# Performance work log

Measured on AMD Instinct MI355X. Metric: run time of the kernel, lower is better.

Reference implementation:

```python
import jax, jax.numpy as jnp
import numpy as np

N = 50000
E = 800000
F_IN = 300
ALPHA = 0.5                      # GCN2Conv alpha
BETA = float(np.log(0.2 / 2.0 + 1.0))  # log(theta/layer + 1), theta=0.2, layer=2
NEG_SLOPE = 0.2                  # GATv2 leaky_relu slope
H, DH = 2, 32                    # GATv2 heads, per-head dim


def _glorot(key, shape):
    s = (6.0 / (shape[0] + shape[-1])) ** 0.5
    return jax.random.uniform(key, shape, jnp.float32, -s, s)


def setup_inputs() -> dict:
    key = jax.random.key(0)
    ks = jax.random.split(key, 24)
    inp = {
        'x': jax.random.normal(ks[0], (N, F_IN), jnp.float32),
        'edge_index': jax.random.randint(ks[1], (2, E), 0, N, dtype=jnp.int32),
        # encoder params
        'W_enc1': _glorot(ks[2], (F_IN, 256)), 'b_enc1': jnp.zeros((256,), jnp.float32),
        'W_enc2': _glorot(ks[3], (256, 256)),                       # GCN2Conv (no bias)
        'W_enc3': _glorot(ks[4], (256, 128)), 'b_enc3': jnp.zeros((128,), jnp.float32),
        'W_enc4': _glorot(ks[5], (128, 64)),  'b_enc4': jnp.zeros((64,), jnp.float32),
        'W_enc5': _glorot(ks[6], (64, 32)),   'b_enc5': jnp.zeros((32,), jnp.float32),
        'Wl_gat': _glorot(ks[7], (32, H * DH)),
        'Wr_gat': _glorot(ks[8], (32, H * DH)),
        'att_gat': _glorot(ks[9], (H, DH)),
        'b_gat': jnp.zeros((H * DH,), jnp.float32),
        # decoder params
        'W_dec1': _glorot(ks[10], (64, 128)),  'b_dec1': jnp.zeros((128,), jnp.float32),
        'W_dec2': _glorot(ks[11], (128, 256)), 'b_dec2': jnp.zeros((256,), jnp.float32),
        'W_dec3': _glorot(ks[12], (256, 256)),                      # GCN2Conv (no bias)
        'W_dec4': _glorot(ks[13], (256, F_IN)), 'b_dec4': jnp.zeros((F_IN,), jnp.float32),
    }
    return inp


def _forward(x, edge_index,
             W_enc1, b_enc1, W_enc2, W_enc3, b_enc3, W_enc4, b_enc4, W_enc5, b_enc5,
             Wl_gat, Wr_gat, att_gat, b_gat,
             W_dec1, b_dec1, W_dec2, b_dec2, W_dec3, W_dec4, b_dec4):
    loops = jnp.arange(N, dtype=edge_index.dtype)
    src = jnp.concatenate([edge_index[0], loops])  # [E+N]
    dst = jnp.concatenate([edge_index[1], loops])
    # symmetric GCN normalization with self-loops (PyG gcn_norm)
    deg = jax.ops.segment_sum(jnp.ones_like(src, jnp.float32), dst, num_segments=N)
    dinv = jnp.where(deg > 0, jax.lax.rsqrt(jnp.maximum(deg, 1e-12)), 0.0)
    norm = dinv[src] * dinv[dst]  # [E+N]

    def prop(h):  # normalized adjacency apply: gather -> scale -> scatter-add
        return jax.ops.segment_sum(h[src] * norm[:, None], dst, num_segments=N)

    def gcn(h, W, b):
        return prop(h @ W) + b

    def gcn2(h, W):  # GCNII with x_0 = layer input, shared weights
        hp = (1.0 - ALPHA) * prop(h) + ALPHA * h
        return (1.0 - BETA) * hp + BETA * (hp @ W)

    def gatv2(h, Wl, Wr, att, b):
        xl = (h @ Wl).reshape(N, H, DH)  # source transform
        xr = (h @ Wr).reshape(N, H, DH)  # target transform
        e = jax.nn.leaky_relu(xl[src] + xr[dst], NEG_SLOPE)  # [E+N, H, DH]
        logits = jnp.einsum('ehd,hd->eh', e, att)            # [E+N, H]
        m = jax.lax.stop_gradient(jax.ops.segment_max(logits, dst, num_segments=N))
        ex = jnp.exp(logits - m[dst])
        den = jax.ops.segment_sum(ex, dst, num_segments=N)
        a = ex / (den[dst] + 1e-16)                          # softmax over in-edges
        out = jax.ops.segment_sum(xl[src] * a[:, :, None], dst, num_segments=N)
        return out.reshape(N, H * DH) + b

    h = gcn(x, W_enc1, b_enc1)
    h = gcn2(h, W_enc2)
    h = gcn(h, W_enc3, b_enc3)
    h = gcn(h, W_enc4, b_enc4)
    h = gcn(h, W_enc5, b_enc5)
    h = gatv2(h, Wl_gat, Wr_gat, att_gat, b_gat)
    h = jax.nn.relu(h)
    h = gcn(h, W_dec1, b_dec1)
    h = gcn(h, W_dec2, b_dec2)
    h = gcn2(h, W_dec3)
    h = gcn(h, W_dec4, b_dec4)
    return jax.nn.sigmoid(h)


def reference(x, edge_index,
              W_enc1, b_enc1, W_enc2, W_enc3, b_enc3, W_enc4, b_enc4, W_enc5, b_enc5,
              Wl_gat, Wr_gat, att_gat, b_gat,
              W_dec1, b_dec1, W_dec2, b_dec2, W_dec3, W_dec4, b_dec4):
    return _forward(x, edge_index,
                    W_enc1, b_enc1, W_enc2, W_enc3, b_enc3, W_enc4, b_enc4, W_enc5, b_enc5,
                    Wl_gat, Wr_gat, att_gat, b_gat,
                    W_dec1, b_dec1, W_dec2, b_dec2, W_dec3, W_dec4, b_dec4)
```

## Files before the change

### kernel.cpp

```cpp
#include <hip/hip_runtime.h>
#include <math.h>

#define NN 50000
#define FIN 300
#define SS 304
constexpr float ALPHA_C = 0.5f;
constexpr float BETA_C  = 0.09531017980432486f;
constexpr float NEG_SLOPE = 0.2f;

typedef unsigned short u16;
typedef __attribute__((ext_vector_type(8))) short short8;
typedef __attribute__((ext_vector_type(4))) float f32x4;
typedef _Float16 hf4 __attribute__((ext_vector_type(4)));

__global__ void hist_kernel(const int* __restrict__ dst, int* __restrict__ deg, int E) {
    int e = blockIdx.x * blockDim.x + threadIdx.x;
    if (e < E) atomicAdd(&deg[dst[e]], 1);
}

__global__ void scan_kernel(const int* __restrict__ deg, int* __restrict__ rowptr, int n) {
    __shared__ int sh[1024];
    __shared__ int carry;
    if (threadIdx.x == 0) { carry = 0; rowptr[0] = 0; }
    __syncthreads();
    for (int base = 0; base < n; base += 1024) {
        int i = base + threadIdx.x;
        int v = (i < n) ? deg[i] : 0;
        sh[threadIdx.x] = v;
        __syncthreads();
        for (int off = 1; off < 1024; off <<= 1) {
            int t = (threadIdx.x >= off) ? sh[threadIdx.x - off] : 0;
            __syncthreads();
            sh[threadIdx.x] += t;
            __syncthreads();
        }
        if (i < n) rowptr[i + 1] = sh[threadIdx.x] + carry;
        __syncthreads();
        if (threadIdx.x == 0) carry += sh[1023];
        __syncthreads();
    }
}

__global__ void dinv_kernel(const int* __restrict__ deg, float* __restrict__ dinv, int n) {
    int i = blockIdx.x * blockDim.x + threadIdx.x;
    if (i < n) dinv[i] = rsqrtf((float)deg[i] + 1.0f);
}

__global__ void copy_int_kernel(const int* __restrict__ a, int* __restrict__ b, int n) {
    int i = blockIdx.x * blockDim.x + threadIdx.x;
    if (i < n) b[i] = a[i];
}

__global__ void fill_kernel(const int* __restrict__ src, const int* __restrict__ dst,
                            const float* __restrict__ dinv, int* __restrict__ cursor,
                            int* __restrict__ csr_src, float* __restrict__ csr_w, int E) {
    int e = blockIdx.x * blockDim.x + threadIdx.x;
    if (e < E) {
        int s = src[e], d = dst[e];
        int p = atomicAdd(&cursor[d], 1);
        csr_src[p] = s;
        csr_w[p]   = dinv[s] * dinv[d];
    }
}

__global__ void splitw_kernel(const float* __restrict__ W, u16* __restrict__ WhT,
                              u16* __restrict__ WlT, int K, int M, int Kp, int total) {
    int t = blockIdx.x * blockDim.x + threadIdx.x;
    if (t >= total) return;
    int c = t / Kp, k = t - c * Kp;
    float x = (c < M && k < K) ? W[(size_t)k * M + c] : 0.f;
    unsigned u = __float_as_uint(x);
    WhT[t] = (u16)(u >> 16);
    float lo = x - __uint_as_float(u & 0xFFFF0000u);
    WlT[t] = (u16)(__float_as_uint(lo) >> 16);
}

__global__ __launch_bounds__(256)
void gemm_mfma_kernel(const float* __restrict__ A, const u16* __restrict__ WhT,
                      const u16* __restrict__ WlT, float* __restrict__ C,
                      _Float16* __restrict__ Cs, int n, int K, int M, int Kp,
                      float cAB, float cA, const float* __restrict__ bias, int gx) {
    __shared__ u16 sAh[64 * 40], sAl[64 * 40], sWh[64 * 40], sWl[64 * 40];
    const int tid = threadIdx.x;
    const int nwg = gridDim.x;
    const int q = nwg >> 3, r = nwg & 7;
    const int xcd = blockIdx.x & 7, off = blockIdx.x >> 3;
    const int wgid = (xcd < r ? xcd * (q + 1) : r * (q + 1) + (xcd - r) * q) + off;
    const int colBase = (wgid % gx) * 64;
    const int rowBase = (wgid / gx) * 64;
    const int lane = tid & 63, wid = tid >> 6;
    const int wr = (wid >> 1) * 32, wc = (wid & 1) * 32;
    const int fr = lane & 15, ko = (lane >> 4) * 8;
    const int wsc = tid >> 2, wsk = (tid & 3) * 8;

    f32x4 acc[2][2] = {};

    for (int k0 = 0; k0 < Kp; k0 += 32) {
        {
            size_t g = (size_t)(colBase + wsc) * Kp + k0 + wsk;
            *(uint4*)&sWh[wsc * 40 + wsk] = *(const uint4*)&WhT[g];
            *(uint4*)&sWl[wsc * 40 + wsk] = *(const uint4*)&WlT[g];
        }
        const bool fullk = (k0 + 32 <= K);
        for (int s = tid; s < 512; s += 256) {
            int rr = s >> 3, kb = (s & 7) * 4;
            int gr = rowBase + rr, kk = k0 + kb;
            float x0 = 0.f, x1 = 0.f, x2 = 0.f, x3 = 0.f;
            if (gr < n) {
                const float* ap = A + (size_t)gr * K + kk;
                if (fullk) { float4 v = *(const float4*)ap; x0 = v.x; x1 = v.y; x2 = v.z; x3 = v.w; }
                else {
                    if (kk     < K) x0 = ap[0];
                    if (kk + 1 < K) x1 = ap[1];
                    if (kk + 2 < K) x2 = ap[2];
                    if (kk + 3 < K) x3 = ap[3];
                }
            }
            unsigned u0 = __float_as_uint(x0), u1 = __float_as_uint(x1);
            unsigned u2 = __float_as_uint(x2), u3 = __float_as_uint(x3);
            uint2 hp; hp.x = (u1 & 0xFFFF0000u) | (u0 >> 16);
                      hp.y = (u3 & 0xFFFF0000u) | (u2 >> 16);
            float l0 = x0 - __uint_as_float(u0 & 0xFFFF0000u);
            float l1 = x1 - __uint_as_float(u1 & 0xFFFF0000u);
            float l2 = x2 - __uint_as_float(u2 & 0xFFFF0000u);
            float l3 = x3 - __uint_as_float(u3 & 0xFFFF0000u);
            uint2 lp; lp.x = (__float_as_uint(l1) & 0xFFFF0000u) | (__float_as_uint(l0) >> 16);
                      lp.y = (__float_as_uint(l3) & 0xFFFF0000u) | (__float_as_uint(l2) >> 16);
            *(uint2*)&sAh[rr * 40 + kb] = hp;
            *(uint2*)&sAl[rr * 40 + kb] = lp;
        }
        __syncthreads();

        short8 ah[2], al[2], bh[2], bl[2];
        ah[0] = *(const short8*)&sAh[(wr +      fr) * 40 + ko];
        ah[1] = *(const short8*)&sAh[(wr + 16 + fr) * 40 + ko];
        al[0] = *(const short8*)&sAl[(wr +      fr) * 40 + ko];
        al[1] = *(const short8*)&sAl[(wr + 16 + fr) * 40 + ko];
        bh[0] = *(const short8*)&sWh[(wc +      fr) * 40 + ko];
        bh[1] = *(const short8*)&sWh[(wc + 16 + fr) * 40 + ko];
        bl[0] = *(const short8*)&sWl[(wc +      fr) * 40 + ko];
        bl[1] = *(const short8*)&sWl[(wc + 16 + fr) * 40 + ko];
#pragma unroll
        for (int i = 0; i < 2; i++)
#pragma unroll
            for (int j = 0; j < 2; j++) {
                acc[i][j] = __builtin_amdgcn_mfma_f32_16x16x32_bf16(al[i], bh[j], acc[i][j], 0, 0, 0);
                acc[i][j] = __builtin_amdgcn_mfma_f32_16x16x32_bf16(ah[i], bl[j], acc[i][j], 0, 0, 0);
                acc[i][j] = __builtin_amdgcn_mfma_f32_16x16x32_bf16(ah[i], bh[j], acc[i][j], 0, 0, 0);
            }
        __syncthreads();
    }

#pragma unroll
    for (int i = 0; i < 2; i++)
#pragma unroll
        for (int j = 0; j < 2; j++) {
            int row0 = rowBase + wr + i * 16 + (lane >> 4) * 4;
            int col  = colBase + wc + j * 16 + fr;
            if (col >= M) continue;
            float bv = bias ? bias[col] : 0.f;
#pragma unroll
            for (int qq = 0; qq < 4; qq++) {
                int rr = row0 + qq;
                if (rr >= n) break;
                float v = cAB * acc[i][j][qq] + bv;
                if (cA != 0.f) v += cA * A[(size_t)rr * K + col];
                C[(size_t)rr * M + col] = v;
                if (Cs) Cs[(size_t)rr * SS + col] = (_Float16)v;
            }
        }
}

__global__ __launch_bounds__(256)
void prop_kernel(const float* __restrict__ h, const _Float16* __restrict__ hs,
                 float* __restrict__ out, _Float16* __restrict__ outs,
                 const int* __restrict__ rowptr, const int* __restrict__ csr_src,
                 const float* __restrict__ csr_w, const float* __restrict__ dinv,
                 const float* __restrict__ bias, int n, int D, float cP, float cH) {
    int wv = (blockIdx.x * blockDim.x + threadIdx.x) >> 6;
    int lane = threadIdx.x & 63;
    int D4 = D >> 2;
    int npw = 64 / D4;
    int sub = lane / D4;
    int cl = lane - sub * D4;
    int i = wv * npw + sub;
    if (i >= n) return;
    int c = cl * 4;
    long bi = (long)i * D4 + cl;
    const float4* h4 = (const float4*)h;
    float4 hv = h4[bi];
    float sw = dinv[i] * dinv[i];
    float4 a0 = {sw * hv.x, sw * hv.y, sw * hv.z, sw * hv.w};
    float4 a1 = {0,0,0,0}, a2 = {0,0,0,0}, a3 = {0,0,0,0};
    int p0 = rowptr[i], p1 = rowptr[i + 1];
    int p = p0;
    for (; p + 4 <= p1; p += 4) {
        int s0 = csr_src[p], s1 = csr_src[p+1], s2 = csr_src[p+2], s3 = csr_src[p+3];
        float w0 = csr_w[p], w1 = csr_w[p+1], w2 = csr_w[p+2], w3 = csr_w[p+3];
        hf4 v0 = *(const hf4*)&hs[(size_t)s0 * SS + c];
        hf4 v1 = *(const hf4*)&hs[(size_t)s1 * SS + c];
        hf4 v2 = *(const hf4*)&hs[(size_t)s2 * SS + c];
        hf4 v3 = *(const hf4*)&hs[(size_t)s3 * SS + c];
        a0.x += w0*(float)v0[0]; a0.y += w0*(float)v0[1]; a0.z += w0*(float)v0[2]; a0.w += w0*(float)v0[3];
        a1.x += w1*(float)v1[0]; a1.y += w1*(float)v1[1]; a1.z += w1*(float)v1[2]; a1.w += w1*(float)v1[3];
        a2.x += w2*(float)v2[0]; a2.y += w2*(float)v2[1]; a2.z += w2*(float)v2[2]; a2.w += w2*(float)v2[3];
        a3.x += w3*(float)v3[0]; a3.y += w3*(float)v3[1]; a3.z += w3*(float)v3[2]; a3.w += w3*(float)v3[3];
    }
    for (; p < p1; ++p) {
        int s = csr_src[p];
        float w = csr_w[p];
        hf4 v = *(const hf4*)&hs[(size_t)s * SS + c];
        a0.x += w*(float)v[0]; a0.y += w*(float)v[1]; a0.z += w*(float)v[2]; a0.w += w*(float)v[3];
    }
    float4 acc = {a0.x + a1.x + a2.x + a3.x, a0.y + a1.y + a2.y + a3.y,
                  a0.z + a1.z + a2.z + a3.z, a0.w + a1.w + a2.w + a3.w};
    float4 rr = {cP * acc.x, cP * acc.y, cP * acc.z, cP * acc.w};
    if (cH != 0.f) { rr.x += cH * hv.x; rr.y += cH * hv.y; rr.z += cH * hv.z; rr.w += cH * hv.w; }
    if (bias) { float4 b = ((const float4*)bias)[cl]; rr.x += b.x; rr.y += b.y; rr.z += b.z; rr.w += b.w; }
    ((float4*)out)[bi] = rr;
    if (outs) {
        hf4 o; o[0] = (_Float16)rr.x; o[1] = (_Float16)rr.y; o[2] = (_Float16)rr.z; o[3] = (_Float16)rr.w;
        *(hf4*)&outs[(size_t)i * SS + c] = o;
    }
}

__device__ inline float lrelu(float x) { return x > 0.f ? x : NEG_SLOPE * x; }

__global__ __launch_bounds__(256)
void gat_logits_kernel(const float* __restrict__ xl, const _Float16* __restrict__ xls,
                       const float* __restrict__ xr, const float* __restrict__ att,
                       const int* __restrict__ rowptr, const int* __restrict__ csr_src,
                       float* __restrict__ logits, float* __restrict__ self_logits, int n) {
    int t = blockIdx.x * blockDim.x + threadIdx.x;
    int i = t >> 1, hh = t & 1;
    if (i >= n) return;
    float4 attv[8], xrv[8];
    const float4* att4 = (const float4*)att;
    const float4* xr4 = (const float4*)xr;
#pragma unroll
    for (int c = 0; c < 8; c++) {
        attv[c] = att4[hh * 8 + c];
        xrv[c]  = xr4[(long)i * 16 + hh * 8 + c];
    }
    {
        const float4* xl4 = (const float4*)xl;
        float s = 0.f;
        long b = (long)i * 16 + hh * 8;
#pragma unroll
        for (int c = 0; c < 8; c++) {
            float4 e = xl4[b + c];
            s += lrelu(e.x + xrv[c].x) * attv[c].x;
            s += lrelu(e.y + xrv[c].y) * attv[c].y;
            s += lrelu(e.z + xrv[c].z) * attv[c].z;
            s += lrelu(e.w + xrv[c].w) * attv[c].w;
        }
        self_logits[i * 2 + hh] = s;
    }
    int p0 = rowptr[i], p1 = rowptr[i + 1];
    for (int p = p0; p < p1; ++p) {
        int sn = csr_src[p];
        size_t b = (size_t)sn * SS + hh * 32;
        float s = 0.f;
#pragma unroll
        for (int c = 0; c < 8; c++) {
            hf4 e = *(const hf4*)&xls[b + c * 4];
            s += lrelu((float)e[0] + xrv[c].x) * attv[c].x;
            s += lrelu((float)e[1] + xrv[c].y) * attv[c].y;
            s += lrelu((float)e[2] + xrv[c].z) * attv[c].z;
            s += lrelu((float)e[3] + xrv[c].w) * attv[c].w;
        }
        logits[(long)p * 2 + hh] = s;
    }
}

__global__ __launch_bounds__(256)
void gat_mden_kernel(const float* __restrict__ logits, const float* __restrict__ self_logits,
                     const int* __restrict__ rowptr, float* __restrict__ m_arr,
                     float* __restrict__ den_arr, int n) {
    int t = blockIdx.x * blockDim.x + threadIdx.x;
    int i = t >> 1, hh = t & 1;
    if (i >= n) return;
    int p0 = rowptr[i], p1 = rowptr[i + 1];
    float m = self_logits[i * 2 + hh];
    for (int p = p0; p < p1; ++p) m = fmaxf(m, logits[(long)p * 2 + hh]);
    float den = expf(self_logits[i * 2 + hh] - m);
    for (int p = p0; p < p1; ++p) den += expf(logits[(long)p * 2 + hh] - m);
    m_arr[i * 2 + hh] = m;
    den_arr[i * 2 + hh] = den;
}

__global__ __launch_bounds__(256)
void gat_out_kernel(const float* __restrict__ xl, const _Float16* __restrict__ xls,
                    const int* __restrict__ rowptr, const int* __restrict__ csr_src,
                    const float* __restrict__ logits, const float* __restrict__ self_logits,
                    const float* __restrict__ m_arr, const float* __restrict__ den_arr,
                    const float* __restrict__ bias, float* __restrict__ out,
                    _Float16* __restrict__ outs, int n) {
    int i = (blockIdx.x * blockDim.x + threadIdx.x) >> 6;
    int lane = threadIdx.x & 63;
    if (i >= n) return;
    int hh = lane >> 5;
    float m = m_arr[i * 2 + hh];
    float inv = 1.f / (den_arr[i * 2 + hh] + 1e-16f);
    float acc = expf(self_logits[i * 2 + hh] - m) * inv * xl[(long)i * 64 + lane];
    int p0 = rowptr[i], p1 = rowptr[i + 1];
    for (int p = p0; p < p1; ++p) {
        float w = expf(logits[(long)p * 2 + hh] - m) * inv;
        acc += w * (float)xls[(size_t)csr_src[p] * SS + lane];
    }
    float r = fmaxf(acc + bias[lane], 0.f);
    out[(long)i * 64 + lane] = r;
    outs[(size_t)i * SS + lane] = (_Float16)r;
}

__global__ void sigmoid_kernel(const float* __restrict__ in, float* __restrict__ out, int n4) {
    int i = blockIdx.x * blockDim.x + threadIdx.x;
    if (i < n4) {
        float4 v = ((const float4*)in)[i];
        float4 r;
        r.x = 1.f / (1.f + expf(-v.x));
        r.y = 1.f / (1.f + expf(-v.y));
        r.z = 1.f / (1.f + expf(-v.z));
        r.w = 1.f / (1.f + expf(-v.w));
        ((float4*)out)[i] = r;
    }
}

extern "C" void kernel_launch(void* const* d_in, const int* in_sizes, int n_in,
                              void* d_out, int out_size, void* d_ws, size_t ws_size,
                              hipStream_t stream) {
    const int N = NN;
    const int E = in_sizes[1] / 2;

    struct WSpec { int idx; int K, M; };
    const WSpec wspec[11] = {
        {2, 300, 256},
        {4, 256, 256},
        {5, 256, 128},
        {7, 128, 64},
        {9, 64, 32},
        {11, 32, 64},
        {12, 32, 64},
        {15, 64, 128},
        {17, 128, 256},
        {19, 256, 256},
        {20, 256, 300},
    };
    size_t arena_elems = 0;
    int kp[11], mp[11];
    size_t woff[11];
    for (int i = 0; i < 11; i++) {
        kp[i] = (wspec[i].K + 31) & ~31;
        mp[i] = (wspec[i].M + 63) & ~63;
        woff[i] = arena_elems;
        arena_elems += (size_t)2 * mp[i] * kp[i];
    }

    size_t need = 0;
    need += (size_t)N * 304 * 4 * 2;
    need += (size_t)N * SS * 2;
    need += (size_t)E * 4;
    need += (size_t)E * 2 * 4;
    need += (size_t)N * 2 * 4 * 3;
    need += (size_t)N * 4;
    need += (size_t)N * 4;
    need += (size_t)(N + 4) * 4;
    need += (size_t)N * 4;
    need += (size_t)E * 4;
    need += arena_elems * 2 + 128;
    if (ws_size < need) return;

    const float* x      = (const float*)d_in[0];
    const int*   ei     = (const int*)d_in[1];
    const int*   e_src  = ei;
    const int*   e_dst  = ei + E;
    const float* b1  = (const float*)d_in[3];
    const float* b3  = (const float*)d_in[6];
    const float* b4  = (const float*)d_in[8];
    const float* b5  = (const float*)d_in[10];
    const float* attw= (const float*)d_in[13];
    const float* bg  = (const float*)d_in[14];
    const float* bd1 = (const float*)d_in[16];
    const float* bd2 = (const float*)d_in[18];
    const float* bd4 = (const float*)d_in[21];

    char* w = (char*)d_ws;
    float* bufA = (float*)w;                 w += (size_t)N * 304 * 4;
    float* bufB = (float*)w;                 w += (size_t)N * 304 * 4;
    _Float16* S = (_Float16*)w;              w += (size_t)N * SS * 2;
    float* csr_w = (float*)w;                w += (size_t)E * 4;
    float* logits = (float*)w;               w += (size_t)E * 2 * 4;
    float* self_logits = (float*)w;          w += (size_t)N * 2 * 4;
    float* m_arr = (float*)w;                w += (size_t)N * 2 * 4;
    float* den_arr = (float*)w;              w += (size_t)N * 2 * 4;
    float* dinv = (float*)w;                 w += (size_t)N * 4;
    int* deg = (int*)w;                      w += (size_t)N * 4;
    int* rowptr = (int*)w;                   w += (size_t)(N + 4) * 4;
    int* cursor = (int*)w;                   w += (size_t)N * 4;
    int* csr_src = (int*)w;                  w += (size_t)E * 4;
    w = (char*)(((size_t)w + 63) & ~(size_t)63);
    u16* arena = (u16*)w;                    w += arena_elems * 2;
    float* T = (float*)d_out;

    int nb_e = (E + 255) / 256;
    int nb_n = (N + 255) / 256;
    int nb_wave = (N + 3) / 4;
    int nb_2n = (2 * N + 255) / 256;

    for (int i = 0; i < 11; i++) {
        int total = mp[i] * kp[i];
        splitw_kernel<<<(total + 255) / 256, 256, 0, stream>>>(
            (const float*)d_in[wspec[i].idx], arena + woff[i], arena + woff[i] + total,
            wspec[i].K, wspec[i].M, kp[i], total);
    }

    hipMemsetAsync(deg, 0, (size_t)N * 4, stream);
    hist_kernel<<<nb_e, 256, 0, stream>>>(e_dst, deg, E);
    scan_kernel<<<1, 1024, 0, stream>>>(deg, rowptr, N);
    dinv_kernel<<<nb_n, 256, 0, stream>>>(deg, dinv, N);
    copy_int_kernel<<<nb_n, 256, 0, stream>>>(rowptr, cursor, N);
    fill_kernel<<<nb_e, 256, 0, stream>>>(e_src, e_dst, dinv, cursor, csr_src, csr_w, E);

    auto gemm = [&](int wi, const float* A, float* C, float cAB, float cA,
                    const float* bias, bool shadow) {
        int K = wspec[wi].K, M = wspec[wi].M;
        int total = mp[wi] * kp[wi];
        int gx = (M + 63) / 64, gy = (N + 63) / 64;
        gemm_mfma_kernel<<<gx * gy, 256, 0, stream>>>(
            A, arena + woff[wi], arena + woff[wi] + total, C, shadow ? S : nullptr,
            N, K, M, kp[wi], cAB, cA, bias, gx);
    };
    auto prop = [&](const float* h, float* out, int D, float cP, float cH,
                    const float* bias, bool shadow) {
        int npw = 64 / (D >> 2);
        int npb = 4 * npw;
        int nb = (N + npb - 1) / npb;
        prop_kernel<<<nb, 256, 0, stream>>>(h, S, out, shadow ? S : nullptr,
                                            rowptr, csr_src, csr_w, dinv,
                                            bias, N, D, cP, cH);
    };

    gemm(0, x, T, 1.f, 0.f, nullptr, true);
    prop(T, bufA, 256, 1.f, 0.f, b1, true);
    prop(bufA, bufB, 256, 1.f - ALPHA_C, ALPHA_C, nullptr, false);
    gemm(1, bufB, bufA, BETA_C, 1.f - BETA_C, nullptr, false);
    gemm(2, bufA, T, 1.f, 0.f, nullptr, true);
    prop(T, bufB, 128, 1.f, 0.f, b3, false);
    gemm(3, bufB, T, 1.f, 0.f, nullptr, true);
    prop(T, bufA, 64, 1.f, 0.f, b4, false);
    gemm(4, bufA, T, 1.f, 0.f, nullptr, true);
    prop(T, bufB, 32, 1.f, 0.f, b5, false);
    gemm(5, bufB, bufA, 1.f, 0.f, nullptr, true);
    gemm(6, bufB, T, 1.f, 0.f, nullptr, false);
    gat_logits_kernel<<<nb_2n, 256, 0, stream>>>(bufA, S, T, attw, rowptr, csr_src,
                                                 logits, self_logits, N);
    gat_mden_kernel<<<nb_2n, 256, 0, stream>>>(logits, self_logits, rowptr, m_arr, den_arr, N);
    gat_out_kernel<<<nb_wave, 256, 0, stream>>>(bufA, S, rowptr, csr_src, logits, self_logits,
                                                m_arr, den_arr, bg, bufB, S, N);
    prop(bufB, bufA, 64, 1.f, 0.f, nullptr, false);
    gemm(7, bufA, T, 1.f, 0.f, bd1, true);
    prop(T, bufB, 128, 1.f, 0.f, nullptr, false);
    gemm(8, bufB, bufA, 1.f, 0.f, bd2, true);
    prop(bufA, bufB, 256, 1.f - ALPHA_C, ALPHA_C, nullptr, false);
    gemm(9, bufB, bufA, BETA_C, 1.f - BETA_C, nullptr, true);
    prop(bufA, bufB, 256, 1.f, 0.f, nullptr, false);
    gemm(10, bufB, T, 1.f, 0.f, bd4, false);
    sigmoid_kernel<<<(out_size / 4 + 255) / 256, 256, 0, stream>>>(T, (float*)d_out, out_size / 4);
}
```

Before: 1.326 ms.

## Store intermediate activations as pre-split bf16 hi/lo pairs to skip in-GEMM splitting

Intermediate activations are now stored as separate bf16 high and low halves with stride 256, written directly by the prop, GEMM and GAT kernels. A new GEMM variant loads these pre-split operands straight into shared memory, so it no longer converts fp32 to bf16 on every tile load. It also uses a 128x64 tile. The fp16 gather shadow buffer is double-buffered (S0/S1), and its stride drops from 304 to 256. The intent is to cut conversion work and the bytes read in the GEMM A path. The cost is an extra u16 array write and read per layer, plus a new tile shape with different occupancy.

```diff
diff --git a/kernel.cpp b/kernel.cpp
--- a/kernel.cpp
+++ b/kernel.cpp
@@ -3,7 +3,8 @@
 
 #define NN 50000
 #define FIN 300
-#define SS 304
+#define PS 256
+#define SHS 256
 constexpr float ALPHA_C = 0.5f;
 constexpr float BETA_C  = 0.09531017980432486f;
 constexpr float NEG_SLOPE = 0.2f;
@@ -12,6 +13,9 @@
 typedef __attribute__((ext_vector_type(8))) short short8;
 typedef __attribute__((ext_vector_type(4))) float f32x4;
 typedef _Float16 hf4 __attribute__((ext_vector_type(4)));
+
+__device__ inline float bfu(u16 u) { return __uint_as_float((unsigned)u << 16); }
+__device__ inline u16 bfhi(float x) { return (u16)(__float_as_uint(x) >> 16); }
 
 __global__ void hist_kernel(const int* __restrict__ dst, int* __restrict__ deg, int E) {
     int e = blockIdx.x * blockDim.x + threadIdx.x;
@@ -69,17 +73,17 @@
     if (t >= total) return;
     int c = t / Kp, k = t - c * Kp;
     float x = (c < M && k < K) ? W[(size_t)k * M + c] : 0.f;
-    unsigned u = __float_as_uint(x);
-    WhT[t] = (u16)(u >> 16);
-    float lo = x - __uint_as_float(u & 0xFFFF0000u);
-    WlT[t] = (u16)(__float_as_uint(lo) >> 16);
+    WhT[t] = bfhi(x);
+    float lo = x - bfu(bfhi(x));
+    WlT[t] = bfhi(lo);
 }
 
 __global__ __launch_bounds__(256)
-void gemm_mfma_kernel(const float* __restrict__ A, const u16* __restrict__ WhT,
-                      const u16* __restrict__ WlT, float* __restrict__ C,
-                      _Float16* __restrict__ Cs, int n, int K, int M, int Kp,
-                      float cAB, float cA, const float* __restrict__ bias, int gx) {
+void gemm_f32a_kernel(const float* __restrict__ A, const u16* __restrict__ WhT,
+                      const u16* __restrict__ WlT, u16* __restrict__ Ch,
+                      u16* __restrict__ Cl, _Float16* __restrict__ Cs,
+                      int n, int K, int M, int Kp,
+                      const float* __restrict__ bias, int gx) {
     __shared__ u16 sAh[64 * 40], sAl[64 * 40], sWh[64 * 40], sWl[64 * 40];
     const int tid = threadIdx.x;
     const int nwg = gridDim.x;
@@ -163,17 +167,107 @@
             for (int qq = 0; qq < 4; qq++) {
                 int rr = row0 + qq;
                 if (rr >= n) break;
+                float v = acc[i][j][qq] + bv;
+                u16 hi = bfhi(v);
+                Ch[(size_t)rr * PS + col] = hi;
+                Cl[(size_t)rr * PS + col] = bfhi(v - bfu(hi));
+                if (Cs) Cs[(size_t)rr * SHS + col] = (_Float16)v;
+            }
+        }
+}
+
+__global__ __launch_bounds__(256)
+void gemm_sp_kernel(const u16* __restrict__ Ah, const u16* __restrict__ Al,
+                    const u16* __restrict__ WhT, const u16* __restrict__ WlT,
+                    float* __restrict__ Cf, u16* __restrict__ Ch, u16* __restrict__ Cl,
+                    _Float16* __restrict__ Cs, int n, int K, int M,
+                    float cAB, float cA, const float* __restrict__ bias, int gx) {
+    __shared__ u16 sAh[128 * 40], sAl[128 * 40], sWh[64 * 40], sWl[64 * 40];
+    const int tid = threadIdx.x;
+    const int nwg = gridDim.x;
+    const int q = nwg >> 3, r = nwg & 7;
+    const int xcd = blockIdx.x & 7, off = blockIdx.x >> 3;
+    const int wgid = (xcd < r ? xcd * (q + 1) : r * (q + 1) + (xcd - r) * q) + off;
+    const int colBase = (wgid % gx) * 64;
+    const int rowBase = (wgid / gx) * 128;
+    const int lane = tid & 63, wid = tid >> 6;
+    const int wr = wid * 32;
+    const int fr = lane & 15, ko = (lane >> 4) * 8;
+    const int wsc = tid >> 2, wsk = (tid & 3) * 8;
+
+    f32x4 acc[2][4] = {};
+
+    for (int k0 = 0; k0 < K; k0 += 32) {
+        {
+            size_t g = (size_t)(colBase + wsc) * K + k0 + wsk;
+            *(uint4*)&sWh[wsc * 40 + wsk] = *(const uint4*)&WhT[g];
+            *(uint4*)&sWl[wsc * 40 + wsk] = *(const uint4*)&WlT[g];
+        }
+#pragma unroll
+        for (int it = 0; it < 2; ++it) {
+            int idx = it * 256 + tid;
+            int rr = idx >> 2, qq = (idx & 3) * 8;
+            int gr = rowBase + rr;
+            uint4 vh = {0, 0, 0, 0}, vl = {0, 0, 0, 0};
+            if (gr < n) {
+                size_t g = (size_t)gr * PS + k0 + qq;
+                vh = *(const uint4*)&Ah[g];
+                vl = *(const uint4*)&Al[g];
+            }
+            *(uint4*)&sAh[rr * 40 + qq] = vh;
+            *(uint4*)&sAl[rr * 40 + qq] = vl;
+        }
+        __syncthreads();
+
+        short8 ah[2], al[2];
+        ah[0] = *(const short8*)&sAh[(wr +      fr) * 40 + ko];
+        ah[1] = *(const short8*)&sAh[(wr + 16 + fr) * 40 + ko];
+        al[0] = *(const short8*)&sAl[(wr +      fr) * 40 + ko];
+        al[1] = *(const short8*)&sAl[(wr + 16 + fr) * 40 + ko];
+#pragma unroll
+        for (int j = 0; j < 4; ++j) {
+            short8 bh = *(const short8*)&sWh[(j * 16 + fr) * 40 + ko];
+            short8 bl = *(const short8*)&sWl[(j * 16 + fr) * 40 + ko];
+#pragma unroll
+            for (int i = 0; i < 2; ++i) {
+                acc[i][j] = __builtin_amdgcn_mfma_f32_16x16x32_bf16(al[i], bh, acc[i][j], 0, 0, 0);
+                acc[i][j] = __builtin_amdgcn_mfma_f32_16x16x32_bf16(ah[i], bl, acc[i][j], 0, 0, 0);
+                acc[i][j] = __builtin_amdgcn_mfma_f32_16x16x32_bf16(ah[i], bh, acc[i][j], 0, 0, 0);
+            }
+        }
+        __syncthreads();
+    }
+
+#pragma unroll
+    for (int i = 0; i < 2; i++)
+#pragma unroll
+        for (int j = 0; j < 4; j++) {
+            int row0 = rowBase + wr + i * 16 + (lane >> 4) * 4;
+            int col  = colBase + j * 16 + fr;
+            if (col >= M) continue;
+            float bv = bias ? bias[col] : 0.f;
+#pragma unroll
+            for (int qq = 0; qq < 4; qq++) {
+                int rr = row0 + qq;
+                if (rr >= n) break;
                 float v = cAB * acc[i][j][qq] + bv;
-                if (cA != 0.f) v += cA * A[(size_t)rr * K + col];
-                C[(size_t)rr * M + col] = v;
-                if (Cs) Cs[(size_t)rr * SS + col] = (_Float16)v;
+                if (cA != 0.f)
+                    v += cA * (bfu(Ah[(size_t)rr * PS + col]) + bfu(Al[(size_t)rr * PS + col]));
+                if (Cf) Cf[(size_t)rr * M + col] = v;
+                if (Ch) {
+                    u16 hi = bfhi(v);
+                    Ch[(size_t)rr * PS + col] = hi;
+                    Cl[(size_t)rr * PS + col] = bfhi(v - bfu(hi));
+                }
+                if (Cs) Cs[(size_t)rr * SHS + col] = (_Float16)v;
             }
         }
 }
 
 __global__ __launch_bounds__(256)
-void prop_kernel(const float* __restrict__ h, const _Float16* __restrict__ hs,
-                 float* __restrict__ out, _Float16* __restrict__ outs,
+void prop_kernel(const u16* __restrict__ Ah, const u16* __restrict__ Al,
+                 const _Float16* __restrict__ hs,
+                 u16* __restrict__ Oh, u16* __restrict__ Ol, _Float16* __restrict__ outs,
                  const int* __restrict__ rowptr, const int* __restrict__ csr_src,
                  const float* __restrict__ csr_w, const float* __restrict__ dinv,
                  const float* __restrict__ bias, int n, int D, float cP, float cH) {
@@ -186,9 +280,10 @@
     int i = wv * npw + sub;
     if (i >= n) return;
     int c = cl * 4;
-    long bi = (long)i * D4 + cl;
-    const float4* h4 = (const float4*)h;
-    float4 hv = h4[bi];
+    ushort4 th = *(const ushort4*)&Ah[(size_t)i * PS + c];
+    ushort4 tl = *(const ushort4*)&Al[(size_t)i * PS + c];
+    float4 hv = {bfu(th.x) + bfu(tl.x), bfu(th.y) + bfu(tl.y),
+                 bfu(th.z) + bfu(tl.z), bfu(th.w) + bfu(tl.w)};
     float sw = dinv[i] * dinv[i];
     float4 a0 = {sw * hv.x, sw * hv.y, sw * hv.z, sw * hv.w};
     float4 a1 = {0,0,0,0}, a2 = {0,0,0,0}, a3 = {0,0,0,0};
@@ -197,10 +292,10 @@
     for (; p + 4 <= p1; p += 4) {
         int s0 = csr_src[p], s1 = csr_src[p+1], s2 = csr_src[p+2], s3 = csr_src[p+3];
         float w0 = csr_w[p], w1 = csr_w[p+1], w2 = csr_w[p+2], w3 = csr_w[p+3];
-        hf4 v0 = *(const hf4*)&hs[(size_t)s0 * SS + c];
-        hf4 v1 = *(const hf4*)&hs[(size_t)s1 * SS + c];
-        hf4 v2 = *(const hf4*)&hs[(size_t)s2 * SS + c];
-        hf4 v3 = *(const hf4*)&hs[(size_t)s3 * SS + c];
+        hf4 v0 = *(const hf4*)&hs[(size_t)s0 * SHS + c];
+        hf4 v1 = *(const hf4*)&hs[(size_t)s1 * SHS + c];
+        hf4 v2 = *(const hf4*)&hs[(size_t)s2 * SHS + c];
+        hf4 v3 = *(const hf4*)&hs[(size_t)s3 * SHS + c];
         a0.x += w0*(float)v0[0]; a0.y += w0*(float)v0[1]; a0.z += w0*(float)v0[2]; a0.w += w0*(float)v0[3];
         a1.x += w1*(float)v1[0]; a1.y += w1*(float)v1[1]; a1.z += w1*(float)v1[2]; a1.w += w1*(float)v1[3];
         a2.x += w2*(float)v2[0]; a2.y += w2*(float)v2[1]; a2.z += w2*(float)v2[2]; a2.w += w2*(float)v2[3];
@@ -209,7 +304,7 @@
     for (; p < p1; ++p) {
         int s = csr_src[p];
         float w = csr_w[p];
-        hf4 v = *(const hf4*)&hs[(size_t)s * SS + c];
+        hf4 v = *(const hf4*)&hs[(size_t)s * SHS + c];
         a0.x += w*(float)v[0]; a0.y += w*(float)v[1]; a0.z += w*(float)v[2]; a0.w += w*(float)v[3];
     }
     float4 acc = {a0.x + a1.x + a2.x + a3.x, a0.y + a1.y + a2.y + a3.y,
@@ -217,17 +312,24 @@
     float4 rr = {cP * acc.x, cP * acc.y, cP * acc.z, cP * acc.w};
     if (cH != 0.f) { rr.x += cH * hv.x; rr.y += cH * hv.y; rr.z += cH * hv.z; rr.w += cH * hv.w; }
     if (bias) { float4 b = ((const float4*)bias)[cl]; rr.x += b.x; rr.y += b.y; rr.z += b.z; rr.w += b.w; }
-    ((float4*)out)[bi] = rr;
+    ushort4 oh, ol;
+    oh.x = bfhi(rr.x); ol.x = bfhi(rr.x - bfu(oh.x));
+    oh.y = bfhi(rr.y); ol.y = bfhi(rr.y - bfu(oh.y));
+    oh.z = bfhi(rr.z); ol.z = bfhi(rr.z - bfu(oh.z));
+    oh.w = bfhi(rr.w); ol.w = bfhi(rr.w - bfu(oh.w));
+    *(ushort4*)&Oh[(size_t)i * PS + c] = oh;
+    *(ushort4*)&Ol[(size_t)i * PS + c] = ol;
     if (outs) {
         hf4 o; o[0] = (_Float16)rr.x; o[1] = (_Float16)rr.y; o[2] = (_Float16)rr.z; o[3] = (_Float16)rr.w;
-        *(hf4*)&outs[(size_t)i * SS + c] = o;
+        *(hf4*)&outs[(size_t)i * SHS + c] = o;
     }
 }
 
 __device__ inline float lrelu(float x) { return x > 0.f ? x : NEG_SLOPE * x; }
 
 __global__ __launch_bounds__(256)
-void gat_logits_kernel(const float* __restrict__ xl, const _Float16* __restrict__ xls,
+void gat_logits_kernel(const u16* __restrict__ xlh, const u16* __restrict__ xll,
+                       const _Float16* __restrict__ xls,
                        const float* __restrict__ xr, const float* __restrict__ att,
                        const int* __restrict__ rowptr, const int* __restrict__ csr_src,
                        float* __restrict__ logits, float* __restrict__ self_logits, int n) {
@@ -243,23 +345,23 @@
         xrv[c]  = xr4[(long)i * 16 + hh * 8 + c];
     }
     {
-        const float4* xl4 = (const float4*)xl;
         float s = 0.f;
-        long b = (long)i * 16 + hh * 8;
+        size_t b = (size_t)i * PS + hh * 32;
 #pragma unroll
         for (int c = 0; c < 8; c++) {
-            float4 e = xl4[b + c];
-            s += lrelu(e.x + xrv[c].x) * attv[c].x;
-            s += lrelu(e.y + xrv[c].y) * attv[c].y;
-            s += lrelu(e.z + xrv[c].z) * attv[c].z;
-            s += lrelu(e.w + xrv[c].w) * attv[c].w;
+            ushort4 eh = *(const ushort4*)&xlh[b + c * 4];
+            ushort4 el = *(const ushort4*)&xll[b + c * 4];
+            s += lrelu(bfu(eh.x) + bfu(el.x) + xrv[c].x) * attv[c].x;
+            s += lrelu(bfu(eh.y) + bfu(el.y) + xrv[c].y) * attv[c].y;
+            s += lrelu(bfu(eh.z) + bfu(el.z) + xrv[c].z) * attv[c].z;
+            s += lrelu(bfu(eh.w) + bfu(el.w) + xrv[c].w) * attv[c].w;
         }
         self_logits[i * 2 + hh] = s;
     }
     int p0 = rowptr[i], p1 = rowptr[i + 1];
     for (int p = p0; p < p1; ++p) {
         int sn = csr_src[p];
-        size_t b = (size_t)sn * SS + hh * 32;
+        size_t b = (size_t)sn * SHS + hh * 32;
         float s = 0.f;
 #pragma unroll
         for (int c = 0; c < 8; c++) {
@@ -290,27 +392,31 @@
 }
 
 __global__ __launch_bounds__(256)
-void gat_out_kernel(const float* __restrict__ xl, const _Float16* __restrict__ xls,
+void gat_out_kernel(const u16* __restrict__ xlh, const u16* __restrict__ xll,
+                    const _Float16* __restrict__ xls,
                     const int* __restrict__ rowptr, const int* __restrict__ csr_src,
                     const float* __restrict__ logits, const float* __restrict__ self_logits,
                     const float* __restrict__ m_arr, const float* __restrict__ den_arr,
-                    const float* __restrict__ bias, float* __restrict__ out,
-                    _Float16* __restrict__ outs, int n) {
+                    const float* __restrict__ bias, u16* __restrict__ Oh,
+                    u16* __restrict__ Ol, _Float16* __restrict__ outs, int n) {
     int i = (blockIdx.x * blockDim.x + threadIdx.x) >> 6;
     int lane = threadIdx.x & 63;
     if (i >= n) return;
     int hh = lane >> 5;
     float m = m_arr[i * 2 + hh];
     float inv = 1.f / (den_arr[i * 2 + hh] + 1e-16f);
-    float acc = expf(self_logits[i * 2 + hh] - m) * inv * xl[(long)i * 64 + lane];
+    float xv = bfu(xlh[(size_t)i * PS + lane]) + bfu(xll[(size_t)i * PS + lane]);
+    float acc = expf(self_logits[i * 2 + hh] - m) * inv * xv;
     int p0 = rowptr[i], p1 = rowptr[i + 1];
     for (int p = p0; p < p1; ++p) {
         float w = expf(logits[(long)p * 2 + hh] - m) * inv;
-        acc += w * (float)xls[(size_t)csr_src[p] * SS + lane];
+        acc += w * (float)xls[(size_t)csr_src[p] * SHS + lane];
     }
     float r = fmaxf(acc + bias[lane], 0.f);
-    out[(long)i * 64 + lane] = r;
-    outs[(size_t)i * SS + lane] = (_Float16)r;
+    u16 hi = bfhi(r);
+    Oh[(size_t)i * PS + lane] = hi;
+    Ol[(size_t)i * PS + lane] = bfhi(r - bfu(hi));
+    outs[(size_t)i * SHS + lane] = (_Float16)r;
 }
 
 __global__ void sigmoid_kernel(const float* __restrict__ in, float* __restrict__ out, int n4) {
@@ -357,15 +463,13 @@
     }
 
     size_t need = 0;
-    need += (size_t)N * 304 * 4 * 2;
-    need += (size_t)N * SS * 2;
+    need += (size_t)N * PS * 2 * 4;
+    need += (size_t)N * SHS * 2 * 2;
     need += (size_t)E * 4;
     need += (size_t)E * 2 * 4;
     need += (size_t)N * 2 * 4 * 3;
-    need += (size_t)N * 4;
-    need += (size_t)N * 4;
+    need += (size_t)N * 4 * 3;
     need += (size_t)(N + 4) * 4;
-    need += (size_t)N * 4;
     need += (size_t)E * 4;
     need += arena_elems * 2 + 128;
     if (ws_size < need) return;
@@ -385,9 +489,12 @@
     const float* bd4 = (const float*)d_in[21];
 
     char* w = (char*)d_ws;
-    float* bufA = (float*)w;                 w += (size_t)N * 304 * 4;
-    float* bufB = (float*)w;                 w += (size_t)N * 304 * 4;
-    _Float16* S = (_Float16*)w;              w += (size_t)N * SS * 2;
+    u16* PAh = (u16*)w;                      w += (size_t)N * PS * 2;
+    u16* PAl = (u16*)w;                      w += (size_t)N * PS * 2;
+    u16* PBh = (u16*)w;                      w += (size_t)N * PS * 2;
+    u16* PBl = (u16*)w;                      w += (size_t)N * PS * 2;
+    _Float16* S0 = (_Float16*)w;             w += (size_t)N * SHS * 2;
+    _Float16* S1 = (_Float16*)w;             w += (size_t)N * SHS * 2;
     float* csr_w = (float*)w;                w += (size_t)E * 4;
     float* logits = (float*)w;               w += (size_t)E * 2 * 4;
     float* self_logits = (float*)w;          w += (size_t)N * 2 * 4;
@@ -421,49 +528,56 @@
     copy_int_kernel<<<nb_n, 256, 0, stream>>>(rowptr, cursor, N);
     fill_kernel<<<nb_e, 256, 0, stream>>>(e_src, e_dst, dinv, cursor, csr_src, csr_w, E);
 
-    auto gemm = [&](int wi, const float* A, float* C, float cAB, float cA,
-                    const float* bias, bool shadow) {
+    auto gemm = [&](int wi, const u16* Ah, const u16* Al, float* Cf, u16* Ch, u16* Cl,
+                    _Float16* Cs, float cAB, float cA, const float* bias) {
         int K = wspec[wi].K, M = wspec[wi].M;
         int total = mp[wi] * kp[wi];
-        int gx = (M + 63) / 64, gy = (N + 63) / 64;
-        gemm_mfma_kernel<<<gx * gy, 256, 0, stream>>>(
-            A, arena + woff[wi], arena + woff[wi] + total, C, shadow ? S : nullptr,
-            N, K, M, kp[wi], cAB, cA, bias, gx);
+        int gx = (M + 63) / 64, gy = (N + 127) / 128;
+        gemm_sp_kernel<<<gx * gy, 256, 0, stream>>>(
+            Ah, Al, arena + woff[wi], arena + woff[wi] + total,
+            Cf, Ch, Cl, Cs, N, K, M, cAB, cA, bias, gx);
     };
-    auto prop = [&](const float* h, float* out, int D, float cP, float cH,
-                    const float* bias, bool shadow) {
+    auto prop = [&](const u16* Ah, const u16* Al, const _Float16* hs,
+                    u16* Oh, u16* Ol, _Float16* outs, int D, float cP, float cH,
+                    const float* bias) {
         int npw = 64 / (D >> 2);
         int npb = 4 * npw;
         int nb = (N + npb - 1) / npb;
-        prop_kernel<<<nb, 256, 0, stream>>>(h, S, out, shadow ? S : nullptr,
+        prop_kernel<<<nb, 256, 0, stream>>>(Ah, Al, hs, Oh, Ol, outs,
                                             rowptr, csr_src, csr_w, dinv,
                                             bias, N, D, cP, cH);
     };
 
-    gemm(0, x, T, 1.f, 0.f, nullptr, true);
-    prop(T, bufA, 256, 1.f, 0.f, b1, true);
-    prop(bufA, bufB, 256, 1.f - ALPHA_C, ALPHA_C, nullptr, false);
-    gemm(1, bufB, bufA, BETA_C, 1.f - BETA_C, nullptr, false);
-    gemm(2, bufA, T, 1.f, 0.f, nullptr, true);
-    prop(T, bufB, 128, 1.f, 0.f, b3, false);
-    gemm(3, bufB, T, 1.f, 0.f, nullptr, true);
-    prop(T, bufA, 64, 1.f, 0.f, b4, false);
-    gemm(4, bufA, T, 1.f, 0.f, nullptr, true);
-    prop(T, bufB, 32, 1.f, 0.f, b5, false);
-    gemm(5, bufB, bufA, 1.f, 0.f, nullptr, true);
-    gemm(6, bufB, T, 1.f, 0.f, nullptr, false);
-    gat_logits_kernel<<<nb_2n, 256, 0, stream>>>(bufA, S, T, attw, rowptr, csr_src,
+    {
+        int gx = (256 + 63) / 64, gy = (N + 63) / 64;
+        gemm_f32a_kernel<<<gx * gy, 256, 0, stream>>>(
+            x, arena + woff[0], arena + woff[0] + mp[0] * kp[0],
+            PAh, PAl, S0, N, 300, 256, kp[0], nullptr, gx);
+    }
+    prop(PAh, PAl, S0, PBh, PBl, S1, 256, 1.f, 0.f, b1);
+    prop(PBh, PBl, S1, PAh, PAl, nullptr, 256, 1.f - ALPHA_C, ALPHA_C, nullptr);
+    gemm(1, PAh, PAl, nullptr, PBh, PBl, nullptr, BETA_C, 1.f - BETA_C, nullptr);
+    gemm(2, PBh, PBl, nullptr, PAh, PAl, S0, 1.f, 0.f, nullptr);
+    prop(PAh, PAl, S0, PBh, PBl, nullptr, 128, 1.f, 0.f, b3);
+    gemm(3, PBh, PBl, nullptr, PAh, PAl, S1, 1.f, 0.f, nullptr);
+    prop(PAh, PAl, S1, PBh, PBl, nullptr, 64, 1.f, 0.f, b4);
+    gemm(4, PBh, PBl, nullptr, PAh, PAl, S0, 1.f, 0.f, nullptr);
+    prop(PAh, PAl, S0, PBh, PBl, nullptr, 32, 1.f, 0.f, b5);
+    gemm(5, PBh, PBl, nullptr, PAh, PAl, S1, 1.f, 0.f, nullptr);
+    gemm(6, PBh, PBl, T, nullptr, nullptr, nullptr, 1.f, 0.f, nullptr);
+    gat_logits_kernel<<<nb_2n, 256, 0, stream>>>(PAh, PAl, S1, T, attw, rowptr, csr_src,
                                                  logits, self_logits, N);
     gat_mden_kernel<<<nb_2n, 256, 0, stream>>>(logits, self_logits, rowptr, m_arr, den_arr, N);
-    gat_out_kernel<<<nb_wave, 256, 0, stream>>>(bufA, S, rowptr, csr_src, logits, self_logits,
-                                                m_arr, den_arr, bg, bufB, S, N);
-    prop(bufB, bufA, 64, 1.f, 0.f, nullptr, false);
-    gemm(7, bufA, T, 1.f, 0.f, bd1, true);
-    prop(T, bufB, 128, 1.f, 0.f, nullptr, false);
-    gemm(8, bufB, bufA, 1.f, 0.f, bd2, true);
-    prop(bufA, bufB, 256, 1.f - ALPHA_C, ALPHA_C, nullptr, false);
-    gemm(9, bufB, bufA, BETA_C, 1.f - BETA_C, nullptr, true);
-    prop(bufA, bufB, 256, 1.f, 0.f, nullptr, false);
-    gemm(10, bufB, T, 1.f, 0.f, bd4, false);
+    gat_out_kernel<<<nb_wave, 256, 0, stream>>>(PAh, PAl, S1, rowptr, csr_src, logits,
+                                                self_logits, m_arr, den_arr, bg,
+                                                PBh, PBl, S0, N);
+    prop(PBh, PBl, S0, PAh, PAl, nullptr, 64, 1.f, 0.f, nullptr);
+    gemm(7, PAh, PAl, nullptr, PBh, PBl, S1, 1.f, 0.f, bd1);
+    prop(PBh, PBl, S1, PAh, PAl, nullptr, 128, 1.f, 0.f, nullptr);
+    gemm(8, PAh, PAl, nullptr, PBh, PBl, S0, 1.f, 0.f, bd2);
+    prop(PBh, PBl, S0, PAh, PAl, nullptr, 256, 1.f - ALPHA_C, ALPHA_C, nullptr);
+    gemm(9, PAh, PAl, nullptr, PBh, PBl, S1, BETA_C, 1.f - BETA_C, nullptr);
+    prop(PBh, PBl, S1, PAh, PAl, nullptr, 256, 1.f, 0.f, nullptr);
+    gemm(10, PAh, PAl, T, nullptr, nullptr, nullptr, 1.f, 0.f, bd4);
     sigmoid_kernel<<<(out_size / 4 + 255) / 256, 256, 0, stream>>>(T, (float*)d_out, out_size / 4);
 }
```

Measured after the change: 1.275 ms. 1.04x faster.
